# Optimization experiments

Hardware: AMD Instinct MI355X
Metric: run time of the kernel (lower is better)

The kernel has to match this reference:

```python
import jax, jax.numpy as jnp
import numpy as np


def _node_layer(X, Z, adj_v, T, W, b, p):
    # d_e = (Z @ p^T): per-edge scalar; multiplier = T diag(d_e) T^T  (Nv,Nv)
    d = (Z @ p.T)[:, 0]
    mult = (T * d[None, :]) @ T.T
    n = mult.shape[0]
    idx = jnp.arange(n)
    M = mult.at[idx, idx].set(1.0)           # diagonal forced to 1
    A = M * adj_v
    A = A / jnp.max(A, axis=0, keepdims=True)  # column-max normalization
    return A @ (X @ W) + b, Z


def _edge_layer(X, Z, adj_e, T, W, b, p):
    # d_v = (X @ p^T): per-node scalar; multiplier = T^T diag(d_v) T  (Ne,Ne)
    d = (X @ p.T)[:, 0]
    mult = (T.T * d[None, :]) @ T
    n = mult.shape[0]
    idx = jnp.arange(n)
    M = mult.at[idx, idx].set(1.0)
    A = M * adj_e
    A = A / jnp.max(A, axis=0, keepdims=True)
    return X, A @ (Z @ W) + b


def setup_inputs() -> dict:
    key = jax.random.key(0)
    ks = jax.random.split(key, 16)
    B, Nv, Ne = 16, 1024, 2048
    Fv, Fe, H, C = 128, 64, 128, 16
    inp = {
        "X": jax.random.normal(ks[0], (B, Nv, Fv), jnp.float32),
        "Z": jax.random.normal(ks[1], (B, Ne, Fe), jnp.float32),
        "adj_e": jax.random.uniform(ks[2], (B, Ne, Ne), jnp.float32, 0.01, 1.0),
        "adj_v": jax.random.uniform(ks[3], (B, Nv, Nv), jnp.float32, 0.01, 1.0),
        "T": jax.random.uniform(ks[4], (B, Nv, Ne), jnp.float32),
        # gc1: node layer  nfeat_v -> nhid, p over edge features
        "W1": jax.random.normal(ks[5], (Fv, H), jnp.float32) * 0.05,
        "b1": jnp.zeros((H,), jnp.float32),
        "p1": jax.random.normal(ks[6], (1, Fe), jnp.float32),
        # gc2: edge layer  nfeat_e -> nfeat_e, p over node features (nhid)
        "W2": jax.random.normal(ks[7], (Fe, Fe), jnp.float32) * 0.05,
        "b2": jnp.zeros((Fe,), jnp.float32),
        "p2": jax.random.normal(ks[8], (1, H), jnp.float32),
        # gc3: node layer  nhid -> nclass
        "W3": jax.random.normal(ks[9], (H, C), jnp.float32) * 0.05,
        "b3": jnp.zeros((C,), jnp.float32),
        "p3": jax.random.normal(ks[10], (1, Fe), jnp.float32),
    }
    return inp


def reference(X, Z, adj_e, adj_v, T, W1, b1, p1, W2, b2, p2, W3, b3, p3):
    # dropout is identity in eval mode
    def single(x, z, ae, av, t):
        x1, z1 = _node_layer(x, z, av, t, W1, b1, p1)
        x1, z1 = jax.nn.relu(x1), jax.nn.relu(z1)
        x2, z2 = _edge_layer(x1, z1, ae, t, W2, b2, p2)
        x2, z2 = jax.nn.relu(x2), jax.nn.relu(z2)
        x3, _ = _node_layer(x2, z2, av, t, W3, b3, p3)
        return x3
    return jax.vmap(single)(X, Z, adj_e, adj_v, T)  # (B, Nv, nclass)
```

## Files before the change

### kernel.cpp

```cpp
#include <hip/hip_runtime.h>
#include <hip/hip_bf16.h>
#include <stdint.h>

#define DEVI __device__ __forceinline__

typedef __bf16 bf16x8_t __attribute__((ext_vector_type(8)));
typedef float f32x4_t __attribute__((ext_vector_type(4)));
typedef unsigned short u16;

static constexpr int NBATCH = 16;
static constexpr int NV = 1024;
static constexpr int NE = 2048;
static constexpr int FV = 128;
static constexpr int FE = 64;
static constexpr int HID = 128;
static constexpr int NCLS = 16;

DEVI u16 f2bf(float f) { __hip_bfloat16 h = __float2bfloat16(f); return *reinterpret_cast<u16*>(&h); }
DEVI float bf2f(u16 u) { union { unsigned int i; float f; } x; x.i = ((unsigned int)u) << 16; return x.f; }

DEVI void gload_lds16(const void* g, void* l) {
  __builtin_amdgcn_global_load_lds(
      (const __attribute__((address_space(1))) unsigned int*)g,
      (__attribute__((address_space(3))) unsigned int*)l, 16, 0, 0);
}

template <bool WRITE_ASC>
__global__ void k_transpose(const float* __restrict__ T, u16* __restrict__ Tbf,
                            u16* __restrict__ Ttbf, const float* __restrict__ d1,
                            u16* __restrict__ Asc1) {
  __shared__ u16 s[32][33];
  const int b = blockIdx.z;
  const int e0 = blockIdx.x * 32, v0 = blockIdx.y * 32;
  const float* Tb = T + (size_t)b * NV * NE;
  u16* T1 = Tbf + (size_t)b * NV * NE;
  u16* T2 = Ttbf + (size_t)b * NE * NV;
  const int tx = threadIdx.x & 31, ty = threadIdx.x >> 5;
  float dv = 0.f;
  if (WRITE_ASC) dv = d1[(size_t)b * NE + e0 + tx];
  #pragma unroll
  for (int i = 0; i < 4; ++i) {
    int v = v0 + ty + i * 8;
    float f = Tb[(size_t)v * NE + e0 + tx];
    u16 u = f2bf(f);
    T1[(size_t)v * NE + e0 + tx] = u;
    if (WRITE_ASC) Asc1[(size_t)b * NV * NE + (size_t)v * NE + e0 + tx] = f2bf(f * dv);
    s[ty + i * 8][tx] = u;
  }
  __syncthreads();
  #pragma unroll
  for (int i = 0; i < 4; ++i) {
    int e = e0 + ty + i * 8;
    T2[(size_t)e * NV + v0 + tx] = s[tx][ty + i * 8];
  }
}

__global__ void k_rowdot(const float* __restrict__ In, const float* __restrict__ p,
                         float* __restrict__ d, int R, int C) {
  const int b = blockIdx.y;
  const int w = threadIdx.x >> 6, l = threadIdx.x & 63;
  const int r = blockIdx.x * 4 + w;
  const float* row = In + ((size_t)b * R + r) * C;
  float s = 0.f;
  for (int c = l; c < C; c += 64) s += row[c] * p[c];
  #pragma unroll
  for (int o = 32; o; o >>= 1) s += __shfl_xor(s, o);
  if (l == 0) d[(size_t)b * R + r] = s;
}

__global__ void k_scale(const u16* __restrict__ In, const float* __restrict__ d,
                        u16* __restrict__ Out, int K, int b0) {
  const int bi = blockIdx.y, bg = b0 + bi;
  const size_t elems = (size_t)NV * NE;
  const size_t idx = ((size_t)blockIdx.x * 256 + threadIdx.x) * 8;
  const float* dd = d + (size_t)bg * K;
  const int k = (int)(idx & (size_t)(K - 1));
  const u16* in = In + (size_t)bg * elems + idx;
  uint4 raw = *(const uint4*)in;
  float f[8];
  f[0] = bf2f(raw.x & 0xffff); f[1] = bf2f(raw.x >> 16);
  f[2] = bf2f(raw.y & 0xffff); f[3] = bf2f(raw.y >> 16);
  f[4] = bf2f(raw.z & 0xffff); f[5] = bf2f(raw.z >> 16);
  f[6] = bf2f(raw.w & 0xffff); f[7] = bf2f(raw.w >> 16);
  u16 o[8];
  #pragma unroll
  for (int t = 0; t < 8; ++t) o[t] = f2bf(f[t] * dd[k + t]);
  *(uint4*)((u16*)Out + (size_t)bi * elems + idx) = *(uint4*)o;
}

__global__ __launch_bounds__(256, 2) void k_gemm128(
    const u16* __restrict__ A, size_t sA, int ldA,
    const u16* __restrict__ Bm, size_t sB, int ldB,
    int M, int K,
    const float* __restrict__ adj, u16* __restrict__ Pout,
    float* __restrict__ pmax, int b0) {
  extern __shared__ __align__(16) char smem[];
  const int gx = gridDim.x, gy = gridDim.y;
  const int total = gx * gy * gridDim.z;
  int orig = blockIdx.x + gx * (blockIdx.y + gy * blockIdx.z);
  const int cpx = total >> 3;
  int swz = (orig & 7) * cpx + (orig >> 3);
  const int bx = swz % gx;
  const int by = (swz / gx) % gy;
  const int bi = swz / (gx * gy);
  const int bg = b0 + bi;

  const u16* Ab = A + (size_t)bi * sA;
  const u16* Bb = Bm + (size_t)bg * sB;
  const int tm = by * 128, tn = bx * 128;
  const int tid = threadIdx.x, wid = tid >> 6, l = tid & 63;
  const int wr = wid >> 1, wc = wid & 1;
  const int lr = l & 15;

  const int srow = tid >> 3;
  const int scol = (((tid & 7) ^ (srow & 7)) << 3);

  const int Lx = (l & 7) << 4;
  const int colb0 = (((l >> 4) << 4)) ^ Lx;
  const int colb1 = (64 + ((l >> 4) << 4)) ^ Lx;
  const int arowb = (wr * 64 + lr) * 128;
  const int browb = (wc * 64 + lr) * 128;

  auto stage = [&](int buf, int k0) {
    char* ab = smem + (buf << 15);
    char* bb = ab + 16384;
    #pragma unroll
    for (int i = 0; i < 4; ++i) {
      gload_lds16(Ab + (size_t)(tm + i * 32 + srow) * ldA + (k0 + scol),
                  ab + i * 4096 + tid * 16);
      gload_lds16(Bb + (size_t)(tn + i * 32 + srow) * ldB + (k0 + scol),
                  bb + i * 4096 + tid * 16);
    }
  };

  f32x4_t acc[4][4];
  const f32x4_t zv = {0.f, 0.f, 0.f, 0.f};
  #pragma unroll
  for (int m = 0; m < 4; ++m)
    #pragma unroll
    for (int n = 0; n < 4; ++n) acc[m][n] = zv;

  const int NT = K >> 6;
  stage(0, 0);
  __syncthreads();

  for (int kt = 0; kt < NT; ++kt) {
    const int buf = kt & 1;
    if (kt + 1 < NT) stage(buf ^ 1, (kt + 1) << 6);
    char* abase = smem + (buf << 15);
    char* bbase = abase + 16384;
    bf16x8_t af[4][2], blo[2][2], bhi[2][2];
    #pragma unroll
    for (int m = 0; m < 4; ++m) {
      af[m][0] = *(const bf16x8_t*)(abase + arowb + m * 2048 + colb0);
      af[m][1] = *(const bf16x8_t*)(abase + arowb + m * 2048 + colb1);
    }
    #pragma unroll
    for (int n = 0; n < 2; ++n) {
      blo[n][0] = *(const bf16x8_t*)(bbase + browb + n * 2048 + colb0);
      blo[n][1] = *(const bf16x8_t*)(bbase + browb + n * 2048 + colb1);
    }
    __builtin_amdgcn_s_setprio(1);
    #pragma unroll
    for (int m = 0; m < 4; ++m)
      #pragma unroll
      for (int n = 0; n < 2; ++n)
        #pragma unroll
        for (int kk = 0; kk < 2; ++kk)
          acc[m][n] = __builtin_amdgcn_mfma_f32_16x16x32_bf16(af[m][kk], blo[n][kk], acc[m][n], 0, 0, 0);
    __builtin_amdgcn_s_setprio(0);
    #pragma unroll
    for (int n = 0; n < 2; ++n) {
      bhi[n][0] = *(const bf16x8_t*)(bbase + browb + (n + 2) * 2048 + colb0);
      bhi[n][1] = *(const bf16x8_t*)(bbase + browb + (n + 2) * 2048 + colb1);
    }
    __builtin_amdgcn_s_setprio(1);
    #pragma unroll
    for (int m = 0; m < 4; ++m)
      #pragma unroll
      for (int n = 0; n < 2; ++n)
        #pragma unroll
        for (int kk = 0; kk < 2; ++kk)
          acc[m][n + 2] = __builtin_amdgcn_mfma_f32_16x16x32_bf16(af[m][kk], bhi[n][kk], acc[m][n + 2], 0, 0, 0);
    __builtin_amdgcn_s_setprio(0);
    __syncthreads();
  }

  const float* adjb = adj + (size_t)bg * M * M;
  u16* Pb = Pout + (size_t)bi * (size_t)M * M;
  float vmax[4] = {0.f, 0.f, 0.f, 0.f};
  #pragma unroll
  for (int m = 0; m < 4; ++m)
    #pragma unroll
    for (int n = 0; n < 4; ++n)
      #pragma unroll
      for (int q = 0; q < 4; ++q) {
        int row = tm + wr * 64 + m * 16 + (l >> 4) * 4 + q;
        int col = tn + wc * 64 + n * 16 + lr;
        float v = acc[m][n][q];
        if (row == col) v = 1.0f;
        v *= adjb[(size_t)row * M + col];
        vmax[n] = fmaxf(vmax[n], v);
        Pb[(size_t)row * M + col] = f2bf(v);
      }
  #pragma unroll
  for (int n = 0; n < 4; ++n) {
    vmax[n] = fmaxf(vmax[n], __shfl_xor(vmax[n], 16));
    vmax[n] = fmaxf(vmax[n], __shfl_xor(vmax[n], 32));
  }
  float* red = (float*)smem;
  if (l < 16) {
    #pragma unroll
    for (int n = 0; n < 4; ++n)
      red[(wid * 4 + n) * 16 + l] = vmax[n];
  }
  __syncthreads();
  if (wr == 0 && l < 16) {
    #pragma unroll
    for (int n = 0; n < 4; ++n) {
      float a = red[(wid * 4 + n) * 16 + l];
      float b = red[((wid + 2) * 4 + n) * 16 + l];
      pmax[((size_t)bi * gy + by) * M + tn + wc * 64 + n * 16 + l] = fmaxf(a, b);
    }
  }
}

__global__ void k_colmax2(const float* __restrict__ pmax, float* __restrict__ c,
                          int N, int G, int b0) {
  const int bi = blockIdx.y, bg = b0 + bi;
  const int j = blockIdx.x * 256 + threadIdx.x;
  const float* pb = pmax + (size_t)bi * G * N;
  float m = 0.f;
  for (int g = 0; g < G; ++g) m = fmaxf(m, pb[(size_t)g * N + j]);
  c[(size_t)bg * N + j] = m;
}

template <int EPI>
__global__ __launch_bounds__(256) void k_gemmPY(
    const u16* __restrict__ A, size_t sA, int ldA,
    const u16* __restrict__ Bm, size_t sB,
    int M, int K, int Ncols,
    const float* __restrict__ bias, float* __restrict__ Fout, int b0) {
  __shared__ __align__(16) u16 As[2][128 * 32];
  __shared__ __align__(16) u16 Bs[2][64 * 32];
  const int bi = blockIdx.z, bg = b0 + bi;
  const u16* Ab = A + (size_t)bi * sA;
  const u16* Bb = Bm + (size_t)bg * sB;
  const int tm = blockIdx.y * 128;
  const int cbase = blockIdx.x * 64;
  const int tid = threadIdx.x, w = tid >> 6, l = tid & 63;
  const int wm = (w >> 1) * 64, wn = (w & 1) * 32;
  const int lr = l & 15, kg = (l >> 4) * 8;
  const int chunk = l & 3;
  int arow[2];
  #pragma unroll
  for (int i = 0; i < 2; ++i) arow[i] = tm + (i * 4 + w) * 16 + (l >> 2);
  int brow = cbase + w * 16 + (l >> 2);
  if (brow >= Ncols) brow = Ncols - 1;

  f32x4_t acc[4][2];
  const f32x4_t zv = {0.f, 0.f, 0.f, 0.f};
  #pragma unroll
  for (int m = 0; m < 4; ++m)
    #pragma unroll
    for (int n = 0; n < 2; ++n) acc[m][n] = zv;

  auto stage = [&](int buf, int k0) {
    #pragma unroll
    for (int i = 0; i < 2; ++i)
      gload_lds16(Ab + (size_t)arow[i] * ldA + k0 + chunk * 8,
                  (char*)As[buf] + (i * 4 + w) * 1024);
    gload_lds16(Bb + (size_t)brow * ldA  + k0 + chunk * 8,
                (char*)Bs[buf] + tid * 16);
  };

  const int nsteps = K >> 5;
  stage(0, 0);
  __syncthreads();
  for (int s = 0; s < nsteps; ++s) {
    const int cur = s & 1;
    if (s + 1 < nsteps) stage(cur ^ 1, (s + 1) << 5);
    bf16x8_t af[4], bfr[2];
    #pragma unroll
    for (int m = 0; m < 4; ++m) af[m] = *(const bf16x8_t*)&As[cur][(wm + m * 16 + lr) * 32 + kg];
    #pragma unroll
    for (int n = 0; n < 2; ++n) bfr[n] = *(const bf16x8_t*)&Bs[cur][(wn + n * 16 + lr) * 32 + kg];
    #pragma unroll
    for (int m = 0; m < 4; ++m)
      #pragma unroll
      for (int n = 0; n < 2; ++n)
        acc[m][n] = __builtin_amdgcn_mfma_f32_16x16x32_bf16(af[m], bfr[n], acc[m][n], 0, 0, 0);
    __syncthreads();
  }

  float* Ob = Fout + (size_t)bg * M * Ncols;
  #pragma unroll
  for (int m = 0; m < 4; ++m)
    #pragma unroll
    for (int n = 0; n < 2; ++n)
      #pragma unroll
      for (int q = 0; q < 4; ++q) {
        int row = tm + wm + m * 16 + (l >> 4) * 4 + q;
        int col = cbase + wn + n * 16 + lr;
        if (col < Ncols) {
          float v = acc[m][n][q] + bias[col];
          if (EPI == 1) v = fmaxf(v, 0.f);
          Ob[(size_t)row * Ncols + col] = v;
        }
      }
}

template <bool RELU_IN>
__global__ __launch_bounds__(256) void k_smallgemm(
    const float* __restrict__ X, size_t sX, int Kd,
    const float* __restrict__ W, int Cc,
    const float* __restrict__ cmax, u16* __restrict__ YT, size_t sY,
    int Nj, int b0) {
  __shared__ float Xs[64][129];
  __shared__ float Ws[128][33];
  const int bg = b0 + blockIdx.y;
  const float* Xb = X + (size_t)bg * sX;
  const int j0 = blockIdx.x * 64;
  const int tid = threadIdx.x;
  for (int idx = tid; idx < 64 * (Kd / 4); idx += 256) {
    int r = idx / (Kd / 4), q = idx % (Kd / 4);
    float4 v = *(const float4*)(Xb + (size_t)(j0 + r) * Kd + q * 4);
    if (RELU_IN) {
      v.x = fmaxf(v.x, 0.f); v.y = fmaxf(v.y, 0.f);
      v.z = fmaxf(v.z, 0.f); v.w = fmaxf(v.w, 0.f);
    }
    Xs[r][q * 4 + 0] = v.x; Xs[r][q * 4 + 1] = v.y;
    Xs[r][q * 4 + 2] = v.z; Xs[r][q * 4 + 3] = v.w;
  }
  const int r = tid & 63, cg = tid >> 6;
  const float rinv = 1.0f / cmax[(size_t)bg * Nj + j0 + r];
  for (int c0 = 0; c0 < Cc; c0 += 32) {
    __syncthreads();
    for (int idx = tid; idx < Kd * 32; idx += 256) {
      int k = idx >> 5, c = c0 + (idx & 31);
      Ws[k][idx & 31] = (c < Cc) ? W[(size_t)k * Cc + c] : 0.f;
    }
    __syncthreads();
    float acc[8] = {0.f, 0.f, 0.f, 0.f, 0.f, 0.f, 0.f, 0.f};
    for (int k = 0; k < Kd; ++k) {
      float xv = Xs[r][k];
      #pragma unroll
      for (int cc = 0; cc < 8; ++cc) acc[cc] += xv * Ws[k][cg * 8 + cc];
    }
    #pragma unroll
    for (int cc = 0; cc < 8; ++cc) {
      int c = c0 + cg * 8 + cc;
      if (c < Cc) YT[(size_t)bg * sY + (size_t)c * Nj + j0 + r] = f2bf(acc[cc] * rinv);
    }
  }
}

extern "C" void kernel_launch(void* const* d_in, const int* in_sizes, int n_in,
                              void* d_out, int out_size, void* d_ws, size_t ws_size,
                              hipStream_t stream) {
  const float* X    = (const float*)d_in[0];
  const float* Z    = (const float*)d_in[1];
  const float* adje = (const float*)d_in[2];
  const float* adjv = (const float*)d_in[3];
  const float* T    = (const float*)d_in[4];
  const float* W1   = (const float*)d_in[5];
  const float* b1   = (const float*)d_in[6];
  const float* p1   = (const float*)d_in[7];
  const float* W2   = (const float*)d_in[8];
  const float* b2   = (const float*)d_in[9];
  const float* p2   = (const float*)d_in[10];
  const float* W3   = (const float*)d_in[11];
  const float* b3   = (const float*)d_in[12];
  const float* p3   = (const float*)d_in[13];
  float* out = (float*)d_out;
  (void)in_sizes; (void)n_in; (void)out_size;

  hipFuncSetAttribute(reinterpret_cast<const void*>(k_gemm128),
                      hipFuncAttributeMaxDynamicSharedMemorySize, 65536);

  char* ws = (char*)d_ws;
  size_t off = 0;
  auto alloc = [&](size_t n) -> char* {
    char* p = ws + off; off = (off + n + 255) & ~(size_t)255; return p;
  };
  u16* Tbf    = (u16*)alloc((size_t)NBATCH * NV * NE * 2);
  u16* Ttbf   = (u16*)alloc((size_t)NBATCH * NE * NV * 2);
  float* dbuf = (float*)alloc((size_t)NBATCH * NE * 4);
  float* cbuf = (float*)alloc((size_t)NBATCH * NE * 4);
  float* pmax = (float*)alloc((size_t)NBATCH * 16 * NE * 4);
  u16* YT     = (u16*)alloc((size_t)NBATCH * NE * 64 * 2);
  float* x1   = (float*)alloc((size_t)NBATCH * NV * HID * 4);
  float* z2   = (float*)alloc((size_t)NBATCH * NE * FE * 4);
  const size_t needA = (size_t)NBATCH * NV * NE * 2;
  const size_t needP = (size_t)NBATCH * NE * NE * 2;
  const bool full = (ws_size >= off + needA + needP + 1024);
  const int nb = full ? NBATCH : 1;
  u16* Asc = (u16*)alloc(full ? needA : (size_t)NV * NE * 2);
  u16* P   = (u16*)alloc(full ? needP : (size_t)NE * NE * 2);

  const dim3 blk(256, 1, 1);

  k_rowdot<<<dim3(NE / 4, NBATCH), blk, 0, stream>>>(Z, p1, dbuf, NE, FE);
  if (full)
    k_transpose<true><<<dim3(NE / 32, NV / 32, NBATCH), blk, 0, stream>>>(
        T, Tbf, Ttbf, dbuf, Asc);
  else
    k_transpose<false><<<dim3(NE / 32, NV / 32, NBATCH), blk, 0, stream>>>(
        T, Tbf, Ttbf, nullptr, nullptr);

  for (int b0 = 0; b0 < NBATCH; b0 += nb) {
    if (!full)
      k_scale<<<dim3((NV * NE) / 2048, nb), blk, 0, stream>>>(Tbf, dbuf, Asc, NE, b0);
    k_gemm128<<<dim3(NV / 128, NV / 128, nb), blk, 65536, stream>>>(
        Asc, (size_t)NV * NE, NE, Tbf, (size_t)NV * NE, NE, NV, NE, adjv, P, pmax, b0);
    k_colmax2<<<dim3(NV / 256, nb), blk, 0, stream>>>(pmax, cbuf, NV, NV / 128, b0);
    k_smallgemm<false><<<dim3(NV / 64, nb), blk, 0, stream>>>(
        X, (size_t)NV * FV, FV, W1, HID, cbuf, YT, (size_t)NV * HID, NV, b0);
    k_gemmPY<1><<<dim3(2, NV / 128, nb), blk, 0, stream>>>(
        P, (size_t)NV * NV, NV, YT, (size_t)NV * HID,
        NV, NV, HID, b1, x1, b0);
  }
  k_rowdot<<<dim3(NV / 4, NBATCH), blk, 0, stream>>>(x1, p2, dbuf, NV, HID);
  for (int b0 = 0; b0 < NBATCH; b0 += nb) {
    k_scale<<<dim3((NE * NV) / 2048, nb), blk, 0, stream>>>(Ttbf, dbuf, Asc, NV, b0);
    k_gemm128<<<dim3(NE / 128, NE / 128, nb), blk, 65536, stream>>>(
        Asc, (size_t)NE * NV, NV, Ttbf, (size_t)NE * NV, NV, NE, NV, adje, P, pmax, b0);
    k_colmax2<<<dim3(NE / 256, nb), blk, 0, stream>>>(pmax, cbuf, NE, NE / 128, b0);
    k_smallgemm<true><<<dim3(NE / 64, nb), blk, 0, stream>>>(
        Z, (size_t)NE * FE, FE, W2, FE, cbuf, YT, (size_t)NE * FE, NE, b0);
    k_gemmPY<1><<<dim3(1, NE / 128, nb), blk, 0, stream>>>(
        P, (size_t)NE * NE, NE, YT, (size_t)NE * FE,
        NE, NE, FE, b2, z2, b0);
  }
  k_rowdot<<<dim3(NE / 4, NBATCH), blk, 0, stream>>>(z2, p3, dbuf, NE, FE);
  for (int b0 = 0; b0 < NBATCH; b0 += nb) {
    k_scale<<<dim3((NV * NE) / 2048, nb), blk, 0, stream>>>(Tbf, dbuf, Asc, NE, b0);
    k_gemm128<<<dim3(NV / 128, NV / 128, nb), blk, 65536, stream>>>(
        Asc, (size_t)NV * NE, NE, Tbf, (size_t)NV * NE, NE, NV, NE, adjv, P, pmax, b0);
    k_colmax2<<<dim3(NV / 256, nb), blk, 0, stream>>>(pmax, cbuf, NV, NV / 128, b0);
    k_smallgemm<false><<<dim3(NV / 64, nb), blk, 0, stream>>>(
        x1, (size_t)NV * HID, HID, W3, NCLS, cbuf, YT, (size_t)NV * NCLS, NV, b0);
    k_gemmPY<2><<<dim3(1, NV / 128, nb), blk, 0, stream>>>(
        P, (size_t)NV * NV, NV, YT, (size_t)NV * NCLS,
        NV, NV, NCLS, b3, out, b0);
  }
}
```

Before: 691.4 us.

## Enlarge adjacency GEMM tile to 256x256 and fold column-max into smallgemm

The multiplier GEMM now uses 256x256 output tiles with 512-thread blocks and 128 KB of double-buffered LDS. Each warp covers 128x64 outputs, which is meant to raise operand reuse and cut global and LDS traffic per MFMA. The separate column-max reduction kernel is removed; smallgemm now reduces the per-tile partial maxima itself, saving a launch and a buffer round trip. The costs are a larger accumulator footprint under a launch bound that asks for two 512-thread blocks per CU, which may force register spills, and LDS use that allows at most one block per CU.

```diff
diff --git a/kernel.cpp b/kernel.cpp
--- a/kernel.cpp
+++ b/kernel.cpp
@@ -88,7 +88,7 @@
   *(uint4*)((u16*)Out + (size_t)bi * elems + idx) = *(uint4*)o;
 }
 
-__global__ __launch_bounds__(256, 2) void k_gemm128(
+__global__ __launch_bounds__(512, 2) void k_gemm256(
     const u16* __restrict__ A, size_t sA, int ldA,
     const u16* __restrict__ Bm, size_t sB, int ldB,
     int M, int K,
@@ -107,10 +107,9 @@
 
   const u16* Ab = A + (size_t)bi * sA;
   const u16* Bb = Bm + (size_t)bg * sB;
-  const int tm = by * 128, tn = bx * 128;
+  const int tm = by * 256, tn = bx * 256;
   const int tid = threadIdx.x, wid = tid >> 6, l = tid & 63;
-  const int wr = wid >> 1, wc = wid & 1;
-  const int lr = l & 15;
+  const int wr = wid >> 2, wc = wid & 3;
 
   const int srow = tid >> 3;
   const int scol = (((tid & 7) ^ (srow & 7)) << 3);
@@ -118,25 +117,25 @@
   const int Lx = (l & 7) << 4;
   const int colb0 = (((l >> 4) << 4)) ^ Lx;
   const int colb1 = (64 + ((l >> 4) << 4)) ^ Lx;
-  const int arowb = (wr * 64 + lr) * 128;
-  const int browb = (wc * 64 + lr) * 128;
+  const int arowb = (wr * 128 + (l & 15)) * 128;
+  const int browb = (wc * 64 + (l & 15)) * 128;
 
   auto stage = [&](int buf, int k0) {
-    char* ab = smem + (buf << 15);
-    char* bb = ab + 16384;
+    char* ab = smem + (buf << 16);
+    char* bb = ab + 32768;
     #pragma unroll
     for (int i = 0; i < 4; ++i) {
-      gload_lds16(Ab + (size_t)(tm + i * 32 + srow) * ldA + (k0 + scol),
-                  ab + i * 4096 + tid * 16);
-      gload_lds16(Bb + (size_t)(tn + i * 32 + srow) * ldB + (k0 + scol),
-                  bb + i * 4096 + tid * 16);
+      gload_lds16(Ab + (size_t)(tm + i * 64 + srow) * ldA + (k0 + scol),
+                  ab + i * 8192 + tid * 16);
+      gload_lds16(Bb + (size_t)(tn + i * 64 + srow) * ldB + (k0 + scol),
+                  bb + i * 8192 + tid * 16);
     }
   };
 
-  f32x4_t acc[4][4];
+  f32x4_t acc[8][4];
   const f32x4_t zv = {0.f, 0.f, 0.f, 0.f};
   #pragma unroll
-  for (int m = 0; m < 4; ++m)
+  for (int m = 0; m < 8; ++m)
     #pragma unroll
     for (int n = 0; n < 4; ++n) acc[m][n] = zv;
 
@@ -147,9 +146,9 @@
   for (int kt = 0; kt < NT; ++kt) {
     const int buf = kt & 1;
     if (kt + 1 < NT) stage(buf ^ 1, (kt + 1) << 6);
-    char* abase = smem + (buf << 15);
-    char* bbase = abase + 16384;
-    bf16x8_t af[4][2], blo[2][2], bhi[2][2];
+    char* abase = smem + (buf << 16);
+    char* bbase = abase + 32768;
+    bf16x8_t af[4][2], bfr[4][2];
     #pragma unroll
     for (int m = 0; m < 4; ++m) {
       af[m][0] = *(const bf16x8_t*)(abase + arowb + m * 2048 + colb0);
@@ -157,8 +156,8 @@
     }
     #pragma unroll
     for (int n = 0; n < 2; ++n) {
-      blo[n][0] = *(const bf16x8_t*)(bbase + browb + n * 2048 + colb0);
-      blo[n][1] = *(const bf16x8_t*)(bbase + browb + n * 2048 + colb1);
+      bfr[n][0] = *(const bf16x8_t*)(bbase + browb + n * 2048 + colb0);
+      bfr[n][1] = *(const bf16x8_t*)(bbase + browb + n * 2048 + colb1);
     }
     __builtin_amdgcn_s_setprio(1);
     #pragma unroll
@@ -167,13 +166,36 @@
       for (int n = 0; n < 2; ++n)
         #pragma unroll
         for (int kk = 0; kk < 2; ++kk)
-          acc[m][n] = __builtin_amdgcn_mfma_f32_16x16x32_bf16(af[m][kk], blo[n][kk], acc[m][n], 0, 0, 0);
+          acc[m][n] = __builtin_amdgcn_mfma_f32_16x16x32_bf16(af[m][kk], bfr[n][kk], acc[m][n], 0, 0, 0);
     __builtin_amdgcn_s_setprio(0);
     #pragma unroll
-    for (int n = 0; n < 2; ++n) {
-      bhi[n][0] = *(const bf16x8_t*)(bbase + browb + (n + 2) * 2048 + colb0);
-      bhi[n][1] = *(const bf16x8_t*)(bbase + browb + (n + 2) * 2048 + colb1);
-    }
+    for (int n = 2; n < 4; ++n) {
+      bfr[n][0] = *(const bf16x8_t*)(bbase + browb + n * 2048 + colb0);
+      bfr[n][1] = *(const bf16x8_t*)(bbase + browb + n * 2048 + colb1);
+    }
+    __builtin_amdgcn_s_setprio(1);
+    #pragma unroll
+    for (int m = 0; m < 4; ++m)
+      #pragma unroll
+      for (int n = 2; n < 4; ++n)
+        #pragma unroll
+        for (int kk = 0; kk < 2; ++kk)
+          acc[m][n] = __builtin_amdgcn_mfma_f32_16x16x32_bf16(af[m][kk], bfr[n][kk], acc[m][n], 0, 0, 0);
+    __builtin_amdgcn_s_setprio(0);
+    #pragma unroll
+    for (int m = 0; m < 4; ++m) {
+      af[m][0] = *(const bf16x8_t*)(abase + arowb + (m + 4) * 2048 + colb0);
+      af[m][1] = *(const bf16x8_t*)(abase + arowb + (m + 4) * 2048 + colb1);
+    }
+    __builtin_amdgcn_s_setprio(1);
+    #pragma unroll
+    for (int m = 0; m < 4; ++m)
+      #pragma unroll
+      for (int n = 2; n < 4; ++n)
+        #pragma unroll
+        for (int kk = 0; kk < 2; ++kk)
+          acc[m + 4][n] = __builtin_amdgcn_mfma_f32_16x16x32_bf16(af[m][kk], bfr[n][kk], acc[m + 4][n], 0, 0, 0);
+    __builtin_amdgcn_s_setprio(0);
     __builtin_amdgcn_s_setprio(1);
     #pragma unroll
     for (int m = 0; m < 4; ++m)
@@ -181,7 +203,7 @@
       for (int n = 0; n < 2; ++n)
         #pragma unroll
         for (int kk = 0; kk < 2; ++kk)
-          acc[m][n + 2] = __builtin_amdgcn_mfma_f32_16x16x32_bf16(af[m][kk], bhi[n][kk], acc[m][n + 2], 0, 0, 0);
+          acc[m + 4][n] = __builtin_amdgcn_mfma_f32_16x16x32_bf16(af[m][kk], bfr[n][kk], acc[m + 4][n], 0, 0, 0);
     __builtin_amdgcn_s_setprio(0);
     __syncthreads();
   }
@@ -190,13 +212,13 @@
   u16* Pb = Pout + (size_t)bi * (size_t)M * M;
   float vmax[4] = {0.f, 0.f, 0.f, 0.f};
   #pragma unroll
-  for (int m = 0; m < 4; ++m)
+  for (int m = 0; m < 8; ++m)
     #pragma unroll
     for (int n = 0; n < 4; ++n)
       #pragma unroll
       for (int q = 0; q < 4; ++q) {
-        int row = tm + wr * 64 + m * 16 + (l >> 4) * 4 + q;
-        int col = tn + wc * 64 + n * 16 + lr;
+        int row = tm + wr * 128 + m * 16 + (l >> 4) * 4 + q;
+        int col = tn + wc * 64 + n * 16 + (l & 15);
         float v = acc[m][n][q];
         if (row == col) v = 1.0f;
         v *= adjb[(size_t)row * M + col];
@@ -212,27 +234,17 @@
   if (l < 16) {
     #pragma unroll
     for (int n = 0; n < 4; ++n)
-      red[(wid * 4 + n) * 16 + l] = vmax[n];
+      red[((wr * 4 + wc) * 4 + n) * 16 + l] = vmax[n];
   }
   __syncthreads();
   if (wr == 0 && l < 16) {
     #pragma unroll
     for (int n = 0; n < 4; ++n) {
-      float a = red[(wid * 4 + n) * 16 + l];
-      float b = red[((wid + 2) * 4 + n) * 16 + l];
+      float a = red[((0 * 4 + wc) * 4 + n) * 16 + l];
+      float b = red[((1 * 4 + wc) * 4 + n) * 16 + l];
       pmax[((size_t)bi * gy + by) * M + tn + wc * 64 + n * 16 + l] = fmaxf(a, b);
     }
   }
-}
-
-__global__ void k_colmax2(const float* __restrict__ pmax, float* __restrict__ c,
-                          int N, int G, int b0) {
-  const int bi = blockIdx.y, bg = b0 + bi;
-  const int j = blockIdx.x * 256 + threadIdx.x;
-  const float* pb = pmax + (size_t)bi * G * N;
-  float m = 0.f;
-  for (int g = 0; g < G; ++g) m = fmaxf(m, pb[(size_t)g * N + j]);
-  c[(size_t)bg * N + j] = m;
 }
 
 template <int EPI>
@@ -314,11 +326,11 @@
 __global__ __launch_bounds__(256) void k_smallgemm(
     const float* __restrict__ X, size_t sX, int Kd,
     const float* __restrict__ W, int Cc,
-    const float* __restrict__ cmax, u16* __restrict__ YT, size_t sY,
+    const float* __restrict__ pmax, int G, u16* __restrict__ YT, size_t sY,
     int Nj, int b0) {
   __shared__ float Xs[64][129];
   __shared__ float Ws[128][33];
-  const int bg = b0 + blockIdx.y;
+  const int bi = blockIdx.y, bg = b0 + bi;
   const float* Xb = X + (size_t)bg * sX;
   const int j0 = blockIdx.x * 64;
   const int tid = threadIdx.x;
@@ -333,7 +345,12 @@
     Xs[r][q * 4 + 2] = v.z; Xs[r][q * 4 + 3] = v.w;
   }
   const int r = tid & 63, cg = tid >> 6;
-  const float rinv = 1.0f / cmax[(size_t)bg * Nj + j0 + r];
+  float mx = 0.f;
+  {
+    const float* pb = pmax + (size_t)bi * G * Nj + (j0 + r);
+    for (int g = 0; g < G; ++g) mx = fmaxf(mx, pb[(size_t)g * Nj]);
+  }
+  const float rinv = 1.0f / mx;
   for (int c0 = 0; c0 < Cc; c0 += 32) {
     __syncthreads();
     for (int idx = tid; idx < Kd * 32; idx += 256) {
@@ -375,8 +392,8 @@
   float* out = (float*)d_out;
   (void)in_sizes; (void)n_in; (void)out_size;
 
-  hipFuncSetAttribute(reinterpret_cast<const void*>(k_gemm128),
-                      hipFuncAttributeMaxDynamicSharedMemorySize, 65536);
+  hipFuncSetAttribute(reinterpret_cast<const void*>(k_gemm256),
+                      hipFuncAttributeMaxDynamicSharedMemorySize, 131072);
 
   char* ws = (char*)d_ws;
   size_t off = 0;
@@ -386,7 +403,6 @@
   u16* Tbf    = (u16*)alloc((size_t)NBATCH * NV * NE * 2);
   u16* Ttbf   = (u16*)alloc((size_t)NBATCH * NE * NV * 2);
   float* dbuf = (float*)alloc((size_t)NBATCH * NE * 4);
-  float* cbuf = (float*)alloc((size_t)NBATCH * NE * 4);
   float* pmax = (float*)alloc((size_t)NBATCH * 16 * NE * 4);
   u16* YT     = (u16*)alloc((size_t)NBATCH * NE * 64 * 2);
   float* x1   = (float*)alloc((size_t)NBATCH * NV * HID * 4);
@@ -399,6 +415,7 @@
   u16* P   = (u16*)alloc(full ? needP : (size_t)NE * NE * 2);
 
   const dim3 blk(256, 1, 1);
+  const dim3 blk512(512, 1, 1);
 
   k_rowdot<<<dim3(NE / 4, NBATCH), blk, 0, stream>>>(Z, p1, dbuf, NE, FE);
   if (full)
@@ -411,11 +428,10 @@
   for (int b0 = 0; b0 < NBATCH; b0 += nb) {
     if (!full)
       k_scale<<<dim3((NV * NE) / 2048, nb), blk, 0, stream>>>(Tbf, dbuf, Asc, NE, b0);
-    k_gemm128<<<dim3(NV / 128, NV / 128, nb), blk, 65536, stream>>>(
+    k_gemm256<<<dim3(NV / 256, NV / 256, nb), blk512, 131072, stream>>>(
         Asc, (size_t)NV * NE, NE, Tbf, (size_t)NV * NE, NE, NV, NE, adjv, P, pmax, b0);
-    k_colmax2<<<dim3(NV / 256, nb), blk, 0, stream>>>(pmax, cbuf, NV, NV / 128, b0);
     k_smallgemm<false><<<dim3(NV / 64, nb), blk, 0, stream>>>(
-        X, (size_t)NV * FV, FV, W1, HID, cbuf, YT, (size_t)NV * HID, NV, b0);
+        X, (size_t)NV * FV, FV, W1, HID, pmax, NV / 256, YT, (size_t)NV * HID, NV, b0);
     k_gemmPY<1><<<dim3(2, NV / 128, nb), blk, 0, stream>>>(
         P, (size_t)NV * NV, NV, YT, (size_t)NV * HID,
         NV, NV, HID, b1, x1, b0);
@@ -423,11 +439,10 @@
   k_rowdot<<<dim3(NV / 4, NBATCH), blk, 0, stream>>>(x1, p2, dbuf, NV, HID);
   for (int b0 = 0; b0 < NBATCH; b0 += nb) {
     k_scale<<<dim3((NE * NV) / 2048, nb), blk, 0, stream>>>(Ttbf, dbuf, Asc, NV, b0);
-    k_gemm128<<<dim3(NE / 128, NE / 128, nb), blk, 65536, stream>>>(
+    k_gemm256<<<dim3(NE / 256, NE / 256, nb), blk512, 131072, stream>>>(
         Asc, (size_t)NE * NV, NV, Ttbf, (size_t)NE * NV, NV, NE, NV, adje, P, pmax, b0);
-    k_colmax2<<<dim3(NE / 256, nb), blk, 0, stream>>>(pmax, cbuf, NE, NE / 128, b0);
     k_smallgemm<true><<<dim3(NE / 64, nb), blk, 0, stream>>>(
-        Z, (size_t)NE * FE, FE, W2, FE, cbuf, YT, (size_t)NE * FE, NE, b0);
+        Z, (size_t)NE * FE, FE, W2, FE, pmax, NE / 256, YT, (size_t)NE * FE, NE, b0);
     k_gemmPY<1><<<dim3(1, NE / 128, nb), blk, 0, stream>>>(
         P, (size_t)NE * NE, NE, YT, (size_t)NE * FE,
         NE, NE, FE, b2, z2, b0);
@@ -435,11 +450,10 @@
   k_rowdot<<<dim3(NE / 4, NBATCH), blk, 0, stream>>>(z2, p3, dbuf, NE, FE);
   for (int b0 = 0; b0 < NBATCH; b0 += nb) {
     k_scale<<<dim3((NV * NE) / 2048, nb), blk, 0, stream>>>(Tbf, dbuf, Asc, NE, b0);
-    k_gemm128<<<dim3(NV / 128, NV / 128, nb), blk, 65536, stream>>>(
+    k_gemm256<<<dim3(NV / 256, NV / 256, nb), blk512, 131072, stream>>>(
         Asc, (size_t)NV * NE, NE, Tbf, (size_t)NV * NE, NE, NV, NE, adjv, P, pmax, b0);
-    k_colmax2<<<dim3(NV / 256, nb), blk, 0, stream>>>(pmax, cbuf, NV, NV / 128, b0);
     k_smallgemm<false><<<dim3(NV / 64, nb), blk, 0, stream>>>(
-        x1, (size_t)NV * HID, HID, W3, NCLS, cbuf, YT, (size_t)NV * NCLS, NV, b0);
+        x1, (size_t)NV * HID, HID, W3, NCLS, pmax, NV / 256, YT, (size_t)NV * NCLS, NV, b0);
     k_gemmPY<2><<<dim3(1, NV / 128, nb), blk, 0, stream>>>(
         P, (size_t)NV * NV, NV, YT, (size_t)NV * NCLS,
         NV, NV, NCLS, b3, out, b0);
```

Measured after the change: 656.4 us. 5.1% less time.
